# Kernel tuning notes

Measured on AMD Instinct MI355X. Metric: run time of the kernel, lower is better.

## Reference

```python
import jax, jax.numpy as jnp
import numpy as np

EPS = 1e-15
CLAMP = 1e-7


def _sqnorm(x):
    return jnp.sum(x * x, axis=-1, keepdims=True)


def _norm(x):
    return jnp.sqrt(jnp.maximum(_sqnorm(x), EPS))


def artanh(x):
    x = jnp.clip(x, -1.0 + CLAMP, 1.0 - CLAMP)
    return 0.5 * (jnp.log1p(x) - jnp.log1p(-x))


def expmap0(u):
    # Poincare ball, c = 1: exp map at origin
    n = _norm(u)
    return jnp.tanh(n) * u / n


def logmap0(p):
    n = _norm(p)
    return artanh(n) * p / n


def mobius_add(x, y):
    x2 = _sqnorm(x)
    y2 = _sqnorm(y)
    xy = jnp.sum(x * y, axis=-1, keepdims=True)
    num = (1.0 + 2.0 * xy + y2) * x + (1.0 - x2) * y
    den = 1.0 + 2.0 * xy + x2 * y2
    return num / jnp.maximum(den, EPS)


def expmap(u, p):
    # exp map of tangent u at ball point p
    n = _norm(u)
    lam = 2.0 / jnp.maximum(1.0 - _sqnorm(p), EPS)
    second = jnp.tanh(0.5 * lam * n) * u / n
    return mobius_add(p, second)


def ptransp0(x, u):
    # parallel transport of tangent u from origin to x: u * (lambda_0 / lambda_x)
    return u * (1.0 - _sqnorm(x))


def setup_inputs() -> dict:
    key = jax.random.key(0)
    k1, k2, k3, k4, k5, k6 = jax.random.split(key, 6)
    n_slot, n_int, d = 30000, 20000, 128
    n_edges, n_rel = 640000, 16
    n_nodes = n_slot + n_int
    return {
        "slot_embed": 0.05 * jax.random.normal(k1, (n_slot, d), dtype=jnp.float32),
        "int_embed": 0.05 * jax.random.normal(k2, (n_int, d), dtype=jnp.float32),
        "relation_embed": 0.05 * jax.random.normal(k3, (n_rel, d), dtype=jnp.float32),
        "src": jax.random.randint(k4, (n_edges,), 0, n_nodes, dtype=jnp.int64) if jax.config.jax_enable_x64 else jax.random.randint(k4, (n_edges,), 0, n_nodes, dtype=jnp.int32),
        "dst": jax.random.randint(k5, (n_edges,), 0, n_nodes, dtype=jnp.int32),
        "edge_type": jax.random.randint(k6, (n_edges,), 0, n_rel, dtype=jnp.int32),
    }


def reference(slot_embed, int_embed, relation_embed, src, dst, edge_type):
    n_slot = slot_embed.shape[0]
    n_nodes = n_slot + int_embed.shape[0]
    embed = jnp.concatenate([slot_embed, int_embed], axis=0)   # 'node'
    node1 = expmap0(embed)                                     # 'node1'

    # per-edge hyperbolic transform: gather src/dst/relation rows
    src_p = node1[src]                          # [E, d] point on ball
    tangent = embed[dst] + relation_embed[edge_type]  # [E, d] tangent at origin
    tan_sum = logmap0(expmap(ptransp0(src_p, tangent), src_p))  # [E, d]

    # g_inv reverses edges, so copy_e + mean aggregates onto original SRC nodes
    sums = jax.ops.segment_sum(tan_sum, src, num_segments=n_nodes)
    cnts = jax.ops.segment_sum(jnp.ones((src.shape[0],), tan_sum.dtype), src,
                               num_segments=n_nodes)
    out = sums / jnp.maximum(cnts, 1.0)[:, None]  # isolated nodes -> 0 (DGL mean)
    return out[:n_slot], out[n_slot:]
```

## Files before the change

### kernel.cpp

```cpp
#include <hip/hip_runtime.h>
#include <math.h>

#define EPSF 1e-15f
#define CLAMPF 1e-7f
#define D 128
#define ELLW 64
#define LOG2E2 2.885390081777927f
#define HALF_LN2 0.34657359027997264f

typedef float v2f __attribute__((ext_vector_type(2)));

__device__ __forceinline__ float rcpf(float x) { return __builtin_amdgcn_rcpf(x); }
__device__ __forceinline__ float rsqf(float x) { return __builtin_amdgcn_rsqf(x); }
__device__ __forceinline__ float exp2h(float x) { return __builtin_amdgcn_exp2f(x); }
__device__ __forceinline__ float log2h(float x) { return __builtin_amdgcn_logf(x); }

__device__ __forceinline__ v2f vfma2(v2f a, v2f b, v2f c) {
#if __has_builtin(__builtin_elementwise_fma)
    return __builtin_elementwise_fma(a, b, c);
#else
    v2f r; r.x = fmaf(a.x, b.x, c.x); r.y = fmaf(a.y, b.y, c.y); return r;
#endif
}

__device__ __forceinline__ float tanh_exp2(float zl) {
    float e2 = exp2h(zl);
    return 1.0f - 2.0f * rcpf(e2 + 1.0f);
}

template<int CTRL>
__device__ __forceinline__ float dpp_add(float v) {
    int s = __builtin_bit_cast(int, v);
    int m = __builtin_amdgcn_update_dpp(s, s, CTRL, 0xF, 0xF, false);
    return v + __builtin_bit_cast(float, m);
}
__device__ __forceinline__ float red16(float v) {
    v = dpp_add<0x128>(v);
    v = dpp_add<0x124>(v);
    v = dpp_add<0x122>(v);
    v = dpp_add<0x121>(v);
    return v;
}

struct v2x2 { v2f lo, hi; };
__device__ __forceinline__ v2x2 ld8(const float* p) {
    float4 f = *(const float4*)p;
    v2x2 r; r.lo = (v2f){f.x, f.y}; r.hi = (v2f){f.z, f.w}; return r;
}

__global__ void build_ell_kernel(const int* __restrict__ src,
                                 const int* __restrict__ dst,
                                 const int* __restrict__ etype,
                                 int* __restrict__ cnt,
                                 int* __restrict__ ell, int n_edges) {
    int i = blockIdx.x * blockDim.x + threadIdx.x;
    int base = i * 4;
    if (base >= n_edges) return;
    if (base + 4 <= n_edges) {
        int4 s = *(const int4*)(src + base);
        int4 d = *(const int4*)(dst + base);
        int4 e = *(const int4*)(etype + base);
        int p;
        p = atomicAdd(cnt + s.x, 1); if (p < ELLW) ell[s.x * ELLW + p] = d.x | (e.x << 20);
        p = atomicAdd(cnt + s.y, 1); if (p < ELLW) ell[s.y * ELLW + p] = d.y | (e.y << 20);
        p = atomicAdd(cnt + s.z, 1); if (p < ELLW) ell[s.z * ELLW + p] = d.z | (e.z << 20);
        p = atomicAdd(cnt + s.w, 1); if (p < ELLW) ell[s.w * ELLW + p] = d.w | (e.w << 20);
    } else {
        for (int k = base; k < n_edges; ++k) {
            int p = atomicAdd(cnt + src[k], 1);
            if (p < ELLW) ell[src[k] * ELLW + p] = dst[k] | (etype[k] << 20);
        }
    }
}

__global__ __launch_bounds__(256)
void node_agg_kernel(const float* __restrict__ slot,
                     const float* __restrict__ intm_virt,
                     const float* __restrict__ rel,
                     const int* __restrict__ ell,
                     const int* __restrict__ cnt,
                     float* __restrict__ out,
                     int n_slot, int n_nodes) {
    int wid  = (blockIdx.x * blockDim.x + threadIdx.x) >> 6;
    int lane = threadIdx.x & 63;
    if (wid >= n_nodes) return;
    int sl = lane & 15;
    int g  = lane >> 4;

    const float* xrow = ((wid < n_slot) ? slot : intm_virt) + (size_t)wid * D + sl * 8;
    v2x2 ea = ld8(xrow);
    v2x2 eb = ld8(xrow + 4);
    v2f ssv = ea.lo * ea.lo;
    ssv = vfma2(ea.hi, ea.hi, ssv);
    ssv = vfma2(eb.lo, eb.lo, ssv);
    ssv = vfma2(eb.hi, eb.hi, ssv);
    float ss = red16(ssv.x + ssv.y);

    float irn = rsqf(fmaxf(ss, EPSF));
    float thn = tanh_exp2(LOG2E2 * ss * irn);
    float tf  = thn * irn;
    float x2  = thn * thn;
    v2f tfv = (v2f){tf, tf};
    v2f x0 = ea.lo * tfv, x1 = ea.hi * tfv;
    v2f x2v_ = eb.lo * tfv, x3 = eb.hi * tfv;

    float fac  = 1.0f - x2;
    float fac2 = fac * fac;

    int cn = cnt[wid];
    int m  = (cn < ELLW) ? cn : ELLW;
    const int* erow = ell + (size_t)wid * ELLW;

    int pk_all = (lane < m) ? erow[lane] : 0;

    float accx = 0.0f;
    v2f ac0 = (v2f){0.f, 0.f}, ac1 = ac0, ac2 = ac0, ac3 = ac0;

    if (m > 0) {
        int pk = __shfl(pk_all, g, 64);
        unsigned di = (unsigned)pk & 0xFFFFF;
        unsigned ri = ((unsigned)pk) >> 20;
        const float* drow = (((int)di < n_slot) ? slot : intm_virt)
                            + (size_t)di * D + sl * 8;
        const float* rrow = rel + (size_t)ri * D + sl * 8;
        v2x2 dA = ld8(drow), dB = ld8(drow + 4);
        v2x2 rA = ld8(rrow), rB = ld8(rrow + 4);

        for (int p = 0; p < m; p += 4) {
            bool ok = (p + g) < m;

            v2f t0 = dA.lo + rA.lo;
            v2f t1 = dA.hi + rA.hi;
            v2f t2 = dB.lo + rB.lo;
            v2f t3 = dB.hi + rB.hi;

            v2f ttv = t0 * t0;
            ttv = vfma2(t1, t1, ttv);
            ttv = vfma2(t2, t2, ttv);
            ttv = vfma2(t3, t3, ttv);
            v2f xtv = x0 * t0;
            xtv = vfma2(x1, t1, xtv);
            xtv = vfma2(x2v_, t2, xtv);
            xtv = vfma2(x3, t3, xtv);

            float tt = red16(ttv.x + ttv.y);
            float xt = red16(xtv.x + xtv.y);

            if (p + 4 < m) {
                int pk2 = __shfl(pk_all, (p + 4 + g) & 63, 64);
                unsigned di2 = (unsigned)pk2 & 0xFFFFF;
                unsigned ri2 = ((unsigned)pk2) >> 20;
                const float* drow2 = (((int)di2 < n_slot) ? slot : intm_virt)
                                     + (size_t)di2 * D + sl * 8;
                const float* rrow2 = rel + (size_t)ri2 * D + sl * 8;
                dA = ld8(drow2); dB = ld8(drow2 + 4);
                rA = ld8(rrow2); rB = ld8(rrow2 + 4);
            }

            float irt = rsqf(fmaxf(tt, EPSF));
            float th  = tanh_exp2(LOG2E2 * tt * irt);
            float w   = th * irt;
            float y2  = th * th;
            float xy  = w * xt;
            float two_xy = xy + xy;
            float opx = 1.0f + two_xy;
            float a   = opx + y2;
            float den = fmaf(x2, y2, opx);
            float invden = rcpf(fmaxf(den, EPSF));
            float poly = fmaf(a * a, x2, fmaf(a * fac, two_xy, fac2 * y2));
            float qq   = invden * invden * poly;
            float irq  = rsqf(fmaxf(qq, EPSF));
            float nq   = qq * irq;
            float cl   = fminf(nq, 1.0f - CLAMPF);
            float at   = HALF_LN2 * log2h((1.0f + cl) * rcpf(1.0f - cl));
            float sc2  = at * irq;
            float k    = sc2 * invden;
            float cx   = k * a;
            float ct   = k * w * fac;
            if (!ok) { cx = 0.0f; ct = 0.0f; }

            accx += cx;
            v2f ctv = (v2f){ct, ct};
            ac0 = vfma2(ctv, t0, ac0);
            ac1 = vfma2(ctv, t1, ac1);
            ac2 = vfma2(ctv, t2, ac2);
            ac3 = vfma2(ctv, t3, ac3);
        }
    }

    v2f axv = (v2f){accx, accx};
    ac0 = vfma2(axv, x0, ac0);
    ac1 = vfma2(axv, x1, ac1);
    ac2 = vfma2(axv, x2v_, ac2);
    ac3 = vfma2(axv, x3, ac3);

    float v0 = ac0.x, v1 = ac0.y, v2 = ac1.x, v3 = ac1.y;
    float v4 = ac2.x, v5 = ac2.y, v6 = ac3.x, v7 = ac3.y;
    #pragma unroll
    for (int d = 16; d < 64; d <<= 1) {
        v0 += __shfl_xor(v0, d, 64);
        v1 += __shfl_xor(v1, d, 64);
        v2 += __shfl_xor(v2, d, 64);
        v3 += __shfl_xor(v3, d, 64);
        v4 += __shfl_xor(v4, d, 64);
        v5 += __shfl_xor(v5, d, 64);
        v6 += __shfl_xor(v6, d, 64);
        v7 += __shfl_xor(v7, d, 64);
    }

    if (lane < 16) {
        float invcnt = rcpf(fmaxf((float)cn, 1.0f));
        float4 w0 = make_float4(v0 * invcnt, v1 * invcnt, v2 * invcnt, v3 * invcnt);
        float4 w1 = make_float4(v4 * invcnt, v5 * invcnt, v6 * invcnt, v7 * invcnt);
        float* orow = out + (size_t)wid * D + sl * 8;
        *(float4*)(orow)     = w0;
        *(float4*)(orow + 4) = w1;
    }
}

extern "C" void kernel_launch(void* const* d_in, const int* in_sizes, int n_in,
                              void* d_out, int out_size, void* d_ws, size_t ws_size,
                              hipStream_t stream) {
    const float* slot = (const float*)d_in[0];
    const float* intm = (const float*)d_in[1];
    const float* rel  = (const float*)d_in[2];
    const int*   src  = (const int*)d_in[3];
    const int*   dst  = (const int*)d_in[4];
    const int*   etyp = (const int*)d_in[5];

    int n_slot  = in_sizes[0] / D;
    int n_int   = in_sizes[1] / D;
    int n_nodes = n_slot + n_int;
    int n_edges = in_sizes[3];

    float* out = (float*)d_out;
    const float* intm_virt = intm - (size_t)n_slot * D;

    int* cnt = (int*)d_ws;
    int* ell = cnt + n_nodes;

    (void)hipMemsetAsync(cnt, 0, (size_t)n_nodes * sizeof(int), stream);

    {
        int threads = 256;
        int nthreads = (n_edges + 3) / 4;
        int blocks = (nthreads + threads - 1) / threads;
        build_ell_kernel<<<blocks, threads, 0, stream>>>(src, dst, etyp, cnt, ell,
                                                         n_edges);
    }
    {
        int threads = 256;
        int blocks = (n_nodes * 64 + threads - 1) / threads;
        node_agg_kernel<<<blocks, threads, 0, stream>>>(slot, intm_virt, rel, ell,
                                                        cnt, out, n_slot, n_nodes);
    }
}
```

Before: 94.58 us.

## Fuse memset, ELL build and aggregation into one cooperative persistent kernel

Replaces the memset plus two kernel launches with a single cooperative kernel that zeroes counts, builds the ELL adjacency with atomics, and aggregates per node, separated by grid-wide syncs. The grid is sized from occupancy, assuming 256 CUs, and waves loop over nodes persistently. The aim is to remove launch overhead and the gaps between kernels. In exchange it adds grid.sync costs, drops the int4 vectorized edge loads, and may lower occupancy or hurt load balance in the aggregation phase.

```diff
diff --git a/kernel.cpp b/kernel.cpp
--- a/kernel.cpp
+++ b/kernel.cpp
@@ -1,5 +1,8 @@
 #include <hip/hip_runtime.h>
+#include <hip/hip_cooperative_groups.h>
 #include <math.h>
+
+namespace cg = cooperative_groups;
 
 #define EPSF 1e-15f
 #define CLAMPF 1e-7f
@@ -48,173 +51,167 @@
     v2x2 r; r.lo = (v2f){f.x, f.y}; r.hi = (v2f){f.z, f.w}; return r;
 }
 
-__global__ void build_ell_kernel(const int* __restrict__ src,
-                                 const int* __restrict__ dst,
-                                 const int* __restrict__ etype,
-                                 int* __restrict__ cnt,
-                                 int* __restrict__ ell, int n_edges) {
-    int i = blockIdx.x * blockDim.x + threadIdx.x;
-    int base = i * 4;
-    if (base >= n_edges) return;
-    if (base + 4 <= n_edges) {
-        int4 s = *(const int4*)(src + base);
-        int4 d = *(const int4*)(dst + base);
-        int4 e = *(const int4*)(etype + base);
-        int p;
-        p = atomicAdd(cnt + s.x, 1); if (p < ELLW) ell[s.x * ELLW + p] = d.x | (e.x << 20);
-        p = atomicAdd(cnt + s.y, 1); if (p < ELLW) ell[s.y * ELLW + p] = d.y | (e.y << 20);
-        p = atomicAdd(cnt + s.z, 1); if (p < ELLW) ell[s.z * ELLW + p] = d.z | (e.z << 20);
-        p = atomicAdd(cnt + s.w, 1); if (p < ELLW) ell[s.w * ELLW + p] = d.w | (e.w << 20);
-    } else {
-        for (int k = base; k < n_edges; ++k) {
-            int p = atomicAdd(cnt + src[k], 1);
-            if (p < ELLW) ell[src[k] * ELLW + p] = dst[k] | (etype[k] << 20);
-        }
+__global__ void fused_kernel(const float* __restrict__ slot,
+                             const float* __restrict__ intm_virt,
+                             const float* __restrict__ rel,
+                             const int* __restrict__ src,
+                             const int* __restrict__ dst,
+                             const int* __restrict__ etyp,
+                             int* __restrict__ cnt,
+                             int* __restrict__ ell,
+                             float* __restrict__ out,
+                             int n_slot, int n_nodes, int n_edges) {
+    cg::grid_group grid = cg::this_grid();
+    int tid  = blockIdx.x * blockDim.x + threadIdx.x;
+    int nthr = gridDim.x * blockDim.x;
+
+    for (int i = tid; i < n_nodes; i += nthr) cnt[i] = 0;
+    grid.sync();
+
+    for (int e = tid; e < n_edges; e += nthr) {
+        int s = src[e];
+        int p = atomicAdd(cnt + s, 1);
+        if (p < ELLW) ell[s * ELLW + p] = dst[e] | (etyp[e] << 20);
     }
-}
-
-__global__ __launch_bounds__(256)
-void node_agg_kernel(const float* __restrict__ slot,
-                     const float* __restrict__ intm_virt,
-                     const float* __restrict__ rel,
-                     const int* __restrict__ ell,
-                     const int* __restrict__ cnt,
-                     float* __restrict__ out,
-                     int n_slot, int n_nodes) {
-    int wid  = (blockIdx.x * blockDim.x + threadIdx.x) >> 6;
-    int lane = threadIdx.x & 63;
-    if (wid >= n_nodes) return;
+    grid.sync();
+
+    int lane = tid & 63;
     int sl = lane & 15;
     int g  = lane >> 4;
-
-    const float* xrow = ((wid < n_slot) ? slot : intm_virt) + (size_t)wid * D + sl * 8;
-    v2x2 ea = ld8(xrow);
-    v2x2 eb = ld8(xrow + 4);
-    v2f ssv = ea.lo * ea.lo;
-    ssv = vfma2(ea.hi, ea.hi, ssv);
-    ssv = vfma2(eb.lo, eb.lo, ssv);
-    ssv = vfma2(eb.hi, eb.hi, ssv);
-    float ss = red16(ssv.x + ssv.y);
-
-    float irn = rsqf(fmaxf(ss, EPSF));
-    float thn = tanh_exp2(LOG2E2 * ss * irn);
-    float tf  = thn * irn;
-    float x2  = thn * thn;
-    v2f tfv = (v2f){tf, tf};
-    v2f x0 = ea.lo * tfv, x1 = ea.hi * tfv;
-    v2f x2v_ = eb.lo * tfv, x3 = eb.hi * tfv;
-
-    float fac  = 1.0f - x2;
-    float fac2 = fac * fac;
-
-    int cn = cnt[wid];
-    int m  = (cn < ELLW) ? cn : ELLW;
-    const int* erow = ell + (size_t)wid * ELLW;
-
-    int pk_all = (lane < m) ? erow[lane] : 0;
-
-    float accx = 0.0f;
-    v2f ac0 = (v2f){0.f, 0.f}, ac1 = ac0, ac2 = ac0, ac3 = ac0;
-
-    if (m > 0) {
-        int pk = __shfl(pk_all, g, 64);
-        unsigned di = (unsigned)pk & 0xFFFFF;
-        unsigned ri = ((unsigned)pk) >> 20;
-        const float* drow = (((int)di < n_slot) ? slot : intm_virt)
-                            + (size_t)di * D + sl * 8;
-        const float* rrow = rel + (size_t)ri * D + sl * 8;
-        v2x2 dA = ld8(drow), dB = ld8(drow + 4);
-        v2x2 rA = ld8(rrow), rB = ld8(rrow + 4);
-
-        for (int p = 0; p < m; p += 4) {
-            bool ok = (p + g) < m;
-
-            v2f t0 = dA.lo + rA.lo;
-            v2f t1 = dA.hi + rA.hi;
-            v2f t2 = dB.lo + rB.lo;
-            v2f t3 = dB.hi + rB.hi;
-
-            v2f ttv = t0 * t0;
-            ttv = vfma2(t1, t1, ttv);
-            ttv = vfma2(t2, t2, ttv);
-            ttv = vfma2(t3, t3, ttv);
-            v2f xtv = x0 * t0;
-            xtv = vfma2(x1, t1, xtv);
-            xtv = vfma2(x2v_, t2, xtv);
-            xtv = vfma2(x3, t3, xtv);
-
-            float tt = red16(ttv.x + ttv.y);
-            float xt = red16(xtv.x + xtv.y);
-
-            if (p + 4 < m) {
-                int pk2 = __shfl(pk_all, (p + 4 + g) & 63, 64);
-                unsigned di2 = (unsigned)pk2 & 0xFFFFF;
-                unsigned ri2 = ((unsigned)pk2) >> 20;
-                const float* drow2 = (((int)di2 < n_slot) ? slot : intm_virt)
-                                     + (size_t)di2 * D + sl * 8;
-                const float* rrow2 = rel + (size_t)ri2 * D + sl * 8;
-                dA = ld8(drow2); dB = ld8(drow2 + 4);
-                rA = ld8(rrow2); rB = ld8(rrow2 + 4);
+    int wave0  = tid >> 6;
+    int nwaves = nthr >> 6;
+
+    for (int wid = wave0; wid < n_nodes; wid += nwaves) {
+        const float* xrow = ((wid < n_slot) ? slot : intm_virt)
+                            + (size_t)wid * D + sl * 8;
+        v2x2 ea = ld8(xrow);
+        v2x2 eb = ld8(xrow + 4);
+        v2f ssv = ea.lo * ea.lo;
+        ssv = vfma2(ea.hi, ea.hi, ssv);
+        ssv = vfma2(eb.lo, eb.lo, ssv);
+        ssv = vfma2(eb.hi, eb.hi, ssv);
+        float ss = red16(ssv.x + ssv.y);
+
+        float irn = rsqf(fmaxf(ss, EPSF));
+        float thn = tanh_exp2(LOG2E2 * ss * irn);
+        float tf  = thn * irn;
+        float x2  = thn * thn;
+        v2f tfv = (v2f){tf, tf};
+        v2f x0 = ea.lo * tfv, x1 = ea.hi * tfv;
+        v2f x2v_ = eb.lo * tfv, x3 = eb.hi * tfv;
+
+        float fac  = 1.0f - x2;
+        float fac2 = fac * fac;
+
+        int cn = cnt[wid];
+        int m  = (cn < ELLW) ? cn : ELLW;
+        const int* erow = ell + (size_t)wid * ELLW;
+
+        int pk_all = (lane < m) ? erow[lane] : 0;
+
+        float accx = 0.0f;
+        v2f ac0 = (v2f){0.f, 0.f}, ac1 = ac0, ac2 = ac0, ac3 = ac0;
+
+        if (m > 0) {
+            int pk = __shfl(pk_all, g, 64);
+            unsigned di = (unsigned)pk & 0xFFFFF;
+            unsigned ri = ((unsigned)pk) >> 20;
+            const float* drow = (((int)di < n_slot) ? slot : intm_virt)
+                                + (size_t)di * D + sl * 8;
+            const float* rrow = rel + (size_t)ri * D + sl * 8;
+            v2x2 dA = ld8(drow), dB = ld8(drow + 4);
+            v2x2 rA = ld8(rrow), rB = ld8(rrow + 4);
+
+            for (int p = 0; p < m; p += 4) {
+                bool ok = (p + g) < m;
+
+                v2f t0 = dA.lo + rA.lo;
+                v2f t1 = dA.hi + rA.hi;
+                v2f t2 = dB.lo + rB.lo;
+                v2f t3 = dB.hi + rB.hi;
+
+                v2f ttv = t0 * t0;
+                ttv = vfma2(t1, t1, ttv);
+                ttv = vfma2(t2, t2, ttv);
+                ttv = vfma2(t3, t3, ttv);
+                v2f xtv = x0 * t0;
+                xtv = vfma2(x1, t1, xtv);
+                xtv = vfma2(x2v_, t2, xtv);
+                xtv = vfma2(x3, t3, xtv);
+
+                float tt = red16(ttv.x + ttv.y);
+                float xt = red16(xtv.x + xtv.y);
+
+                if (p + 4 < m) {
+                    int pk2 = __shfl(pk_all, (p + 4 + g) & 63, 64);
+                    unsigned di2 = (unsigned)pk2 & 0xFFFFF;
+                    unsigned ri2 = ((unsigned)pk2) >> 20;
+                    const float* drow2 = (((int)di2 < n_slot) ? slot : intm_virt)
+                                         + (size_t)di2 * D + sl * 8;
+                    const float* rrow2 = rel + (size_t)ri2 * D + sl * 8;
+                    dA = ld8(drow2); dB = ld8(drow2 + 4);
+                    rA = ld8(rrow2); rB = ld8(rrow2 + 4);
+                }
+
+                float irt = rsqf(fmaxf(tt, EPSF));
+                float th  = tanh_exp2(LOG2E2 * tt * irt);
+                float w   = th * irt;
+                float y2  = th * th;
+                float xy  = w * xt;
+                float two_xy = xy + xy;
+                float opx = 1.0f + two_xy;
+                float a   = opx + y2;
+                float den = fmaf(x2, y2, opx);
+                float invden = rcpf(fmaxf(den, EPSF));
+                float poly = fmaf(a * a, x2, fmaf(a * fac, two_xy, fac2 * y2));
+                float qq   = invden * invden * poly;
+                float irq  = rsqf(fmaxf(qq, EPSF));
+                float nq   = qq * irq;
+                float cl   = fminf(nq, 1.0f - CLAMPF);
+                float at   = HALF_LN2 * log2h((1.0f + cl) * rcpf(1.0f - cl));
+                float sc2  = at * irq;
+                float k    = sc2 * invden;
+                float cx   = k * a;
+                float ct   = k * w * fac;
+                if (!ok) { cx = 0.0f; ct = 0.0f; }
+
+                accx += cx;
+                v2f ctv = (v2f){ct, ct};
+                ac0 = vfma2(ctv, t0, ac0);
+                ac1 = vfma2(ctv, t1, ac1);
+                ac2 = vfma2(ctv, t2, ac2);
+                ac3 = vfma2(ctv, t3, ac3);
             }
-
-            float irt = rsqf(fmaxf(tt, EPSF));
-            float th  = tanh_exp2(LOG2E2 * tt * irt);
-            float w   = th * irt;
-            float y2  = th * th;
-            float xy  = w * xt;
-            float two_xy = xy + xy;
-            float opx = 1.0f + two_xy;
-            float a   = opx + y2;
-            float den = fmaf(x2, y2, opx);
-            float invden = rcpf(fmaxf(den, EPSF));
-            float poly = fmaf(a * a, x2, fmaf(a * fac, two_xy, fac2 * y2));
-            float qq   = invden * invden * poly;
-            float irq  = rsqf(fmaxf(qq, EPSF));
-            float nq   = qq * irq;
-            float cl   = fminf(nq, 1.0f - CLAMPF);
-            float at   = HALF_LN2 * log2h((1.0f + cl) * rcpf(1.0f - cl));
-            float sc2  = at * irq;
-            float k    = sc2 * invden;
-            float cx   = k * a;
-            float ct   = k * w * fac;
-            if (!ok) { cx = 0.0f; ct = 0.0f; }
-
-            accx += cx;
-            v2f ctv = (v2f){ct, ct};
-            ac0 = vfma2(ctv, t0, ac0);
-            ac1 = vfma2(ctv, t1, ac1);
-            ac2 = vfma2(ctv, t2, ac2);
-            ac3 = vfma2(ctv, t3, ac3);
         }
-    }
-
-    v2f axv = (v2f){accx, accx};
-    ac0 = vfma2(axv, x0, ac0);
-    ac1 = vfma2(axv, x1, ac1);
-    ac2 = vfma2(axv, x2v_, ac2);
-    ac3 = vfma2(axv, x3, ac3);
-
-    float v0 = ac0.x, v1 = ac0.y, v2 = ac1.x, v3 = ac1.y;
-    float v4 = ac2.x, v5 = ac2.y, v6 = ac3.x, v7 = ac3.y;
-    #pragma unroll
-    for (int d = 16; d < 64; d <<= 1) {
-        v0 += __shfl_xor(v0, d, 64);
-        v1 += __shfl_xor(v1, d, 64);
-        v2 += __shfl_xor(v2, d, 64);
-        v3 += __shfl_xor(v3, d, 64);
-        v4 += __shfl_xor(v4, d, 64);
-        v5 += __shfl_xor(v5, d, 64);
-        v6 += __shfl_xor(v6, d, 64);
-        v7 += __shfl_xor(v7, d, 64);
-    }
-
-    if (lane < 16) {
-        float invcnt = rcpf(fmaxf((float)cn, 1.0f));
-        float4 w0 = make_float4(v0 * invcnt, v1 * invcnt, v2 * invcnt, v3 * invcnt);
-        float4 w1 = make_float4(v4 * invcnt, v5 * invcnt, v6 * invcnt, v7 * invcnt);
-        float* orow = out + (size_t)wid * D + sl * 8;
-        *(float4*)(orow)     = w0;
-        *(float4*)(orow + 4) = w1;
+
+        v2f axv = (v2f){accx, accx};
+        ac0 = vfma2(axv, x0, ac0);
+        ac1 = vfma2(axv, x1, ac1);
+        ac2 = vfma2(axv, x2v_, ac2);
+        ac3 = vfma2(axv, x3, ac3);
+
+        float v0 = ac0.x, v1 = ac0.y, v2 = ac1.x, v3 = ac1.y;
+        float v4 = ac2.x, v5 = ac2.y, v6 = ac3.x, v7 = ac3.y;
+        #pragma unroll
+        for (int d = 16; d < 64; d <<= 1) {
+            v0 += __shfl_xor(v0, d, 64);
+            v1 += __shfl_xor(v1, d, 64);
+            v2 += __shfl_xor(v2, d, 64);
+            v3 += __shfl_xor(v3, d, 64);
+            v4 += __shfl_xor(v4, d, 64);
+            v5 += __shfl_xor(v5, d, 64);
+            v6 += __shfl_xor(v6, d, 64);
+            v7 += __shfl_xor(v7, d, 64);
+        }
+
+        if (lane < 16) {
+            float invcnt = rcpf(fmaxf((float)cn, 1.0f));
+            float4 w0 = make_float4(v0 * invcnt, v1 * invcnt, v2 * invcnt, v3 * invcnt);
+            float4 w1 = make_float4(v4 * invcnt, v5 * invcnt, v6 * invcnt, v7 * invcnt);
+            float* orow = out + (size_t)wid * D + sl * 8;
+            *(float4*)(orow)     = w0;
+            *(float4*)(orow + 4) = w1;
+        }
     }
 }
 
@@ -239,19 +236,19 @@
     int* cnt = (int*)d_ws;
     int* ell = cnt + n_nodes;
 
-    (void)hipMemsetAsync(cnt, 0, (size_t)n_nodes * sizeof(int), stream);
-
-    {
-        int threads = 256;
-        int nthreads = (n_edges + 3) / 4;
-        int blocks = (nthreads + threads - 1) / threads;
-        build_ell_kernel<<<blocks, threads, 0, stream>>>(src, dst, etyp, cnt, ell,
-                                                         n_edges);
-    }
-    {
-        int threads = 256;
-        int blocks = (n_nodes * 64 + threads - 1) / threads;
-        node_agg_kernel<<<blocks, threads, 0, stream>>>(slot, intm_virt, rel, ell,
-                                                        cnt, out, n_slot, n_nodes);
-    }
-}
+    int nb = 0;
+    if (hipOccupancyMaxActiveBlocksPerMultiprocessor(&nb, fused_kernel, 256, 0)
+        != hipSuccess || nb <= 0) nb = 4;
+    int grid = nb * 256;
+    int max_useful = (n_nodes * 64 + 255) / 256;
+    if (grid > max_useful) grid = max_useful;
+
+    void* args[] = {
+        (void*)&slot, (void*)&intm_virt, (void*)&rel,
+        (void*)&src, (void*)&dst, (void*)&etyp,
+        (void*)&cnt, (void*)&ell, (void*)&out,
+        (void*)&n_slot, (void*)&n_nodes, (void*)&n_edges
+    };
+    (void)hipLaunchCooperativeKernel((const void*)fused_kernel,
+                                     dim3(grid), dim3(256), args, 0, stream);
+}
```

New measurement: 249.0 us. +163.3%, slower.
